# Performance work log

Hardware: AMD Instinct MI355X
Metric: run time of the kernel (lower is better)

## Reference

```python
import jax, jax.numpy as jnp
import numpy as np

B = 8192       # batch size
D = 64         # embedding dim
NUM_GROUPS = 128
TEMP = 0.05    # temperature (init kwarg)
SCALE = 0.05   # keeps exp(-dist/TEMP) > 0 in fp32 (no underflow)


def setup_inputs() -> dict:
    key = jax.random.key(0)
    k1, k2, k3 = jax.random.split(key, 3)
    text = jax.random.normal(k1, (B, D), dtype=jnp.float32) * SCALE
    image = jax.random.normal(k2, (B, D), dtype=jnp.float32) * SCALE
    groups = jax.random.randint(k3, (B,), 0, NUM_GROUPS, dtype=jnp.int64)
    return {"text_embeddings": text, "image_embeddings": image, "groups": groups}


def reference(text_embeddings, image_embeddings, groups):
    n = groups.shape[0]
    # pairwise L2 distances via ||a||^2 + ||b||^2 - 2ab (avoids [B,B,D] tensor)
    d2 = (jnp.sum(image_embeddings**2, axis=1)[:, None]
          + jnp.sum(text_embeddings**2, axis=1)[None, :]
          - 2.0 * image_embeddings @ text_embeddings.T)
    dist = jnp.sqrt(jnp.maximum(d2, 0.0))          # [B,B] dist(image_i, text_j)
    S = jnp.exp(-dist / TEMP)                      # similarities, all > 0
    same = groups[:, None] == groups[None, :]      # [B,B] group equality
    diagS = jnp.diagonal(S)
    A = jnp.where(same, S, 0.0).sum(axis=1) - diagS   # same-group sum, j != i
    F = A + diagS                                      # same-group sum incl. i
    # the original inner 'if numerator == 0' re-loop fires exactly once unless
    # the j=0 iteration already added something (groups[i]==groups[0] and i!=0)
    idx = jnp.arange(n)
    cond = (groups == groups[0]) & (idx != 0)
    num = jnp.where(cond, A, A + F)
    den = jnp.where(same, 0.0, S).sum(axis=1)          # different-group sum
    valid = (num != 0.0) & (den != 0.0)
    ratio = jnp.where(valid, num, 1.0) / jnp.where(valid, den, 1.0)
    per_i = jnp.where(valid, -jnp.log(ratio), 0.0)
    return per_i.sum() / n
```

## Files before the change

### kernel.cpp

```cpp
#include <hip/hip_runtime.h>
#include <hip/hip_bf16.h>
#include <math.h>

typedef unsigned short u16;
typedef __attribute__((ext_vector_type(8))) short short8;
typedef __attribute__((ext_vector_type(4))) float f32x4;

#define NB 8192
#define ND 64
#define K2     832.5475634f
#define M2K2  -1665.0951268f
#define LN2    0.69314718055994531f

__device__ __forceinline__ float simval2(float d2K) {
    return __builtin_amdgcn_exp2f(-__builtin_amdgcn_sqrtf(fmaxf(d2K, 0.0f)));
}

__global__ __launch_bounds__(256) void snn_prep(
    const float* __restrict__ text, const float* __restrict__ image,
    u16* __restrict__ textBf, u16* __restrict__ imageBf,
    float* __restrict__ normT, float* __restrict__ normI,
    float* __restrict__ diagS, float* __restrict__ sameSum,
    float* __restrict__ totSum, float* __restrict__ out)
{
    const int lane = threadIdx.x & 63;
    const int row  = blockIdx.x * 4 + (threadIdx.x >> 6);
    const int idx  = row * ND + lane;

    float t  = text[idx];
    float im = image[idx];
    __hip_bfloat16 tb = __float2bfloat16(t);
    __hip_bfloat16 ib = __float2bfloat16(im);
    u16 tbits, ibits;
    __builtin_memcpy(&tbits, &tb, 2);
    __builtin_memcpy(&ibits, &ib, 2);
    textBf[idx]  = tbits;
    imageBf[idx] = ibits;

    float nt = t * t;
    float ni = im * im;
    float dp = __bfloat162float(tb) * __bfloat162float(ib);
    #pragma unroll
    for (int m = 32; m >= 1; m >>= 1) {
        nt += __shfl_xor(nt, m, 64);
        ni += __shfl_xor(ni, m, 64);
        dp += __shfl_xor(dp, m, 64);
    }
    if (lane == 0) {
        float snt = K2 * nt;
        float sni = K2 * ni;
        normT[row] = snt;
        normI[row] = sni;
        float d2K = fmaf(M2K2, dp, sni + snt);
        diagS[row] = simval2(d2K);
        sameSum[row] = 0.0f;
        totSum[row]  = 0.0f;
        if (row == 0) out[0] = 0.0f;
    }
}

__global__ __launch_bounds__(256, 2) void snn_main(
    const u16* __restrict__ textBf, const u16* __restrict__ imageBf,
    const float* __restrict__ normT, const float* __restrict__ normI,
    const int* __restrict__ groups,
    float* __restrict__ sameSum, float* __restrict__ totSum)
{
    const int lane = threadIdx.x & 63;
    const int w    = threadIdx.x >> 6;
    const int g    = lane >> 4;
    const int l15  = lane & 15;
    const int rowBase  = blockIdx.x * 128 + w * 32;
    const int colChunk = blockIdx.y * 256;

    short8 aFrag[2][2];
    #pragma unroll
    for (int m = 0; m < 2; ++m)
        #pragma unroll
        for (int kk = 0; kk < 2; ++kk)
            aFrag[m][kk] = *(const short8*)(imageBf +
                (rowBase + m * 16 + l15) * ND + kk * 32 + g * 8);

    float nI[2][4];
    int   gI[2][4];
    #pragma unroll
    for (int m = 0; m < 2; ++m)
        #pragma unroll
        for (int r = 0; r < 4; ++r) {
            int row = rowBase + m * 16 + g * 4 + r;
            nI[m][r] = normI[row];
            gI[m][r] = groups[row];
        }

    float sameAcc[2][4];
    float totAcc[2][4];
    #pragma unroll
    for (int m = 0; m < 2; ++m)
        #pragma unroll
        for (int r = 0; r < 4; ++r) { sameAcc[m][r] = 0.0f; totAcc[m][r] = 0.0f; }

    #pragma unroll
    for (int ct = 0; ct < 2; ++ct) {
        const int colBase = colChunk + ct * 128;

        float nT[8];
        int   gJ[8];
        f32x4 acc[2][8];
        #pragma unroll
        for (int n = 0; n < 8; ++n) {
            const int col = colBase + n * 16 + l15;
            nT[n] = normT[col];
            gJ[n] = groups[col];
            short8 b0 = *(const short8*)(textBf + col * ND + g * 8);
            short8 b1 = *(const short8*)(textBf + col * ND + 32 + g * 8);
            #pragma unroll
            for (int m = 0; m < 2; ++m) {
                acc[m][n] = f32x4{0.f, 0.f, 0.f, 0.f};
                acc[m][n] = __builtin_amdgcn_mfma_f32_16x16x32_bf16(
                                aFrag[m][0], b0, acc[m][n], 0, 0, 0);
                acc[m][n] = __builtin_amdgcn_mfma_f32_16x16x32_bf16(
                                aFrag[m][1], b1, acc[m][n], 0, 0, 0);
            }
        }

        #pragma unroll
        for (int m = 0; m < 2; ++m)
            #pragma unroll
            for (int n = 0; n < 8; ++n) {
                f32x4 c = acc[m][n];
                #pragma unroll
                for (int r = 0; r < 4; ++r) {
                    float d2K = fmaf(M2K2, c[r], nI[m][r] + nT[n]);
                    float s   = simval2(d2K);
                    totAcc[m][r] += s;
                    sameAcc[m][r] += (gI[m][r] == gJ[n]) ? s : 0.0f;
                }
            }
    }

    #pragma unroll
    for (int m = 0; m < 2; ++m)
        #pragma unroll
        for (int r = 0; r < 4; ++r) {
            float sv = sameAcc[m][r];
            float tv = totAcc[m][r];
            #pragma unroll
            for (int mk = 8; mk >= 1; mk >>= 1) {
                sv += __shfl_xor(sv, mk, 64);
                tv += __shfl_xor(tv, mk, 64);
            }
            if (l15 == 0) {
                int row = rowBase + m * 16 + g * 4 + r;
                atomicAdd(&sameSum[row], sv);
                atomicAdd(&totSum[row], tv);
            }
        }
}

__global__ __launch_bounds__(256) void snn_finalize(
    const float* __restrict__ sameSum, const float* __restrict__ totSum,
    const float* __restrict__ diagS, const int* __restrict__ groups,
    float* __restrict__ out)
{
    const int i = blockIdx.x * 256 + threadIdx.x;
    float sameS = sameSum[i];
    float tot   = totSum[i];
    float diag  = diagS[i];
    float A = sameS - diag;
    int g0 = groups[0];
    bool cond = (groups[i] == g0) && (i != 0);
    float num = cond ? A : (A + sameS);
    float den = tot - sameS;
    bool valid = (num != 0.0f) && (den != 0.0f);
    float ratio = (valid ? num : 1.0f) / (valid ? den : 1.0f);
    float per = valid ? (-LN2 * __builtin_amdgcn_logf(ratio)) : 0.0f;

    float v = per;
    #pragma unroll
    for (int mk = 32; mk >= 1; mk >>= 1) v += __shfl_xor(v, mk, 64);
    __shared__ float wsum[4];
    if ((threadIdx.x & 63) == 0) wsum[threadIdx.x >> 6] = v;
    __syncthreads();
    if (threadIdx.x == 0) {
        float s = wsum[0] + wsum[1] + wsum[2] + wsum[3];
        atomicAdd(out, s * (1.0f / 8192.0f));
    }
}

extern "C" void kernel_launch(void* const* d_in, const int* in_sizes, int n_in,
                              void* d_out, int out_size, void* d_ws, size_t ws_size,
                              hipStream_t stream) {
    const float* text  = (const float*)d_in[0];
    const float* image = (const float*)d_in[1];
    const int*   groups = (const int*)d_in[2];
    float* out = (float*)d_out;

    char* ws = (char*)d_ws;
    u16* textBf  = (u16*)ws;
    u16* imageBf = (u16*)(ws + (1 << 20));
    float* normT   = (float*)(ws + (2 << 20));
    float* normI   = normT + NB;
    float* diagS   = normI + NB;
    float* sameSum = diagS + NB;
    float* totSum  = sameSum + NB;

    snn_prep<<<NB / 4, 256, 0, stream>>>(text, image, textBf, imageBf,
                                         normT, normI, diagS, sameSum, totSum, out);
    snn_main<<<dim3(64, 32), 256, 0, stream>>>(textBf, imageBf, normT, normI,
                                               groups, sameSum, totSum);
    snn_finalize<<<NB / 256, 256, 0, stream>>>(sameSum, totSum, diagS, groups, out);
}
```

Baseline: 109.7 us.

## Fuse finalize into main via last-block counter and shrink row tile per wave

The separate finalize kernel is removed. Each main block increments a global completion counter, and the last block to finish computes the per-row loss terms and writes the mean. The main kernel's tiling also changes: each wave now handles 16 rows instead of 32 and loops over 16 column tiles with partial unrolling. The grid doubles along rows, so the B (text) fragments are reused less per load. This removes one launch, but the serial reduction of all 8192 rows now runs on a single block at the end.

```diff
diff --git a/kernel.cpp b/kernel.cpp
--- a/kernel.cpp
+++ b/kernel.cpp
@@ -12,6 +12,10 @@
 #define M2K2  -1665.0951268f
 #define LN2    0.69314718055994531f
 
+#define GRID_X 128
+#define GRID_Y 32
+#define TOTAL_BLOCKS (GRID_X * GRID_Y)
+
 __device__ __forceinline__ float simval2(float d2K) {
     return __builtin_amdgcn_exp2f(-__builtin_amdgcn_sqrtf(fmaxf(d2K, 0.0f)));
 }
@@ -21,7 +25,8 @@
     u16* __restrict__ textBf, u16* __restrict__ imageBf,
     float* __restrict__ normT, float* __restrict__ normI,
     float* __restrict__ diagS, float* __restrict__ sameSum,
-    float* __restrict__ totSum, float* __restrict__ out)
+    float* __restrict__ totSum, unsigned int* __restrict__ doneCnt,
+    float* __restrict__ out)
 {
     const int lane = threadIdx.x & 63;
     const int row  = blockIdx.x * 4 + (threadIdx.x >> 6);
@@ -55,134 +60,107 @@
         diagS[row] = simval2(d2K);
         sameSum[row] = 0.0f;
         totSum[row]  = 0.0f;
-        if (row == 0) out[0] = 0.0f;
+        if (row == 0) { *doneCnt = 0u; out[0] = 0.0f; }
     }
 }
 
 __global__ __launch_bounds__(256, 2) void snn_main(
     const u16* __restrict__ textBf, const u16* __restrict__ imageBf,
     const float* __restrict__ normT, const float* __restrict__ normI,
-    const int* __restrict__ groups,
-    float* __restrict__ sameSum, float* __restrict__ totSum)
+    const int* __restrict__ groups, const float* __restrict__ diagS,
+    float* __restrict__ sameSum, float* __restrict__ totSum,
+    unsigned int* __restrict__ doneCnt, float* __restrict__ out)
 {
     const int lane = threadIdx.x & 63;
     const int w    = threadIdx.x >> 6;
     const int g    = lane >> 4;
     const int l15  = lane & 15;
-    const int rowBase  = blockIdx.x * 128 + w * 32;
+    const int rowBase  = blockIdx.x * 64 + w * 16;
     const int colChunk = blockIdx.y * 256;
 
-    short8 aFrag[2][2];
+    short8 aFrag0 = *(const short8*)(imageBf + (rowBase + l15) * ND + g * 8);
+    short8 aFrag1 = *(const short8*)(imageBf + (rowBase + l15) * ND + 32 + g * 8);
+
+    float nI[4];
+    int   gI[4];
     #pragma unroll
-    for (int m = 0; m < 2; ++m)
-        #pragma unroll
-        for (int kk = 0; kk < 2; ++kk)
-            aFrag[m][kk] = *(const short8*)(imageBf +
-                (rowBase + m * 16 + l15) * ND + kk * 32 + g * 8);
+    for (int r = 0; r < 4; ++r) {
+        int row = rowBase + g * 4 + r;
+        nI[r] = normI[row];
+        gI[r] = groups[row];
+    }
 
-    float nI[2][4];
-    int   gI[2][4];
-    #pragma unroll
-    for (int m = 0; m < 2; ++m)
+    float sameAcc[4] = {0.f, 0.f, 0.f, 0.f};
+    float totAcc[4]  = {0.f, 0.f, 0.f, 0.f};
+
+    #pragma unroll 2
+    for (int n = 0; n < 16; ++n) {
+        const int col = colChunk + n * 16 + l15;
+        float nT = normT[col];
+        int   gJ = groups[col];
+        short8 b0 = *(const short8*)(textBf + col * ND + g * 8);
+        short8 b1 = *(const short8*)(textBf + col * ND + 32 + g * 8);
+        f32x4 acc = {0.f, 0.f, 0.f, 0.f};
+        acc = __builtin_amdgcn_mfma_f32_16x16x32_bf16(aFrag0, b0, acc, 0, 0, 0);
+        acc = __builtin_amdgcn_mfma_f32_16x16x32_bf16(aFrag1, b1, acc, 0, 0, 0);
         #pragma unroll
         for (int r = 0; r < 4; ++r) {
-            int row = rowBase + m * 16 + g * 4 + r;
-            nI[m][r] = normI[row];
-            gI[m][r] = groups[row];
+            float d2K = fmaf(M2K2, acc[r], nI[r] + nT);
+            float s   = simval2(d2K);
+            totAcc[r] += s;
+            sameAcc[r] += (gI[r] == gJ) ? s : 0.0f;
         }
-
-    float sameAcc[2][4];
-    float totAcc[2][4];
-    #pragma unroll
-    for (int m = 0; m < 2; ++m)
-        #pragma unroll
-        for (int r = 0; r < 4; ++r) { sameAcc[m][r] = 0.0f; totAcc[m][r] = 0.0f; }
-
-    #pragma unroll
-    for (int ct = 0; ct < 2; ++ct) {
-        const int colBase = colChunk + ct * 128;
-
-        float nT[8];
-        int   gJ[8];
-        f32x4 acc[2][8];
-        #pragma unroll
-        for (int n = 0; n < 8; ++n) {
-            const int col = colBase + n * 16 + l15;
-            nT[n] = normT[col];
-            gJ[n] = groups[col];
-            short8 b0 = *(const short8*)(textBf + col * ND + g * 8);
-            short8 b1 = *(const short8*)(textBf + col * ND + 32 + g * 8);
-            #pragma unroll
-            for (int m = 0; m < 2; ++m) {
-                acc[m][n] = f32x4{0.f, 0.f, 0.f, 0.f};
-                acc[m][n] = __builtin_amdgcn_mfma_f32_16x16x32_bf16(
-                                aFrag[m][0], b0, acc[m][n], 0, 0, 0);
-                acc[m][n] = __builtin_amdgcn_mfma_f32_16x16x32_bf16(
-                                aFrag[m][1], b1, acc[m][n], 0, 0, 0);
-            }
-        }
-
-        #pragma unroll
-        for (int m = 0; m < 2; ++m)
-            #pragma unroll
-            for (int n = 0; n < 8; ++n) {
-                f32x4 c = acc[m][n];
-                #pragma unroll
-                for (int r = 0; r < 4; ++r) {
-                    float d2K = fmaf(M2K2, c[r], nI[m][r] + nT[n]);
-                    float s   = simval2(d2K);
-                    totAcc[m][r] += s;
-                    sameAcc[m][r] += (gI[m][r] == gJ[n]) ? s : 0.0f;
-                }
-            }
     }
 
     #pragma unroll
-    for (int m = 0; m < 2; ++m)
+    for (int r = 0; r < 4; ++r) {
+        float sv = sameAcc[r];
+        float tv = totAcc[r];
         #pragma unroll
-        for (int r = 0; r < 4; ++r) {
-            float sv = sameAcc[m][r];
-            float tv = totAcc[m][r];
-            #pragma unroll
-            for (int mk = 8; mk >= 1; mk >>= 1) {
-                sv += __shfl_xor(sv, mk, 64);
-                tv += __shfl_xor(tv, mk, 64);
-            }
-            if (l15 == 0) {
-                int row = rowBase + m * 16 + g * 4 + r;
-                atomicAdd(&sameSum[row], sv);
-                atomicAdd(&totSum[row], tv);
-            }
+        for (int mk = 8; mk >= 1; mk >>= 1) {
+            sv += __shfl_xor(sv, mk, 64);
+            tv += __shfl_xor(tv, mk, 64);
         }
-}
+        if (l15 == 0) {
+            int row = rowBase + g * 4 + r;
+            atomicAdd(&sameSum[row], sv);
+            atomicAdd(&totSum[row], tv);
+        }
+    }
 
-__global__ __launch_bounds__(256) void snn_finalize(
-    const float* __restrict__ sameSum, const float* __restrict__ totSum,
-    const float* __restrict__ diagS, const int* __restrict__ groups,
-    float* __restrict__ out)
-{
-    const int i = blockIdx.x * 256 + threadIdx.x;
-    float sameS = sameSum[i];
-    float tot   = totSum[i];
-    float diag  = diagS[i];
-    float A = sameS - diag;
-    int g0 = groups[0];
-    bool cond = (groups[i] == g0) && (i != 0);
-    float num = cond ? A : (A + sameS);
-    float den = tot - sameS;
-    bool valid = (num != 0.0f) && (den != 0.0f);
-    float ratio = (valid ? num : 1.0f) / (valid ? den : 1.0f);
-    float per = valid ? (-LN2 * __builtin_amdgcn_logf(ratio)) : 0.0f;
-
-    float v = per;
-    #pragma unroll
-    for (int mk = 32; mk >= 1; mk >>= 1) v += __shfl_xor(v, mk, 64);
+    __shared__ int lastFlag;
     __shared__ float wsum[4];
-    if ((threadIdx.x & 63) == 0) wsum[threadIdx.x >> 6] = v;
     __syncthreads();
     if (threadIdx.x == 0) {
-        float s = wsum[0] + wsum[1] + wsum[2] + wsum[3];
-        atomicAdd(out, s * (1.0f / 8192.0f));
+        __threadfence();
+        unsigned int old = atomicAdd(doneCnt, 1u);
+        lastFlag = (old == TOTAL_BLOCKS - 1) ? 1 : 0;
+    }
+    __syncthreads();
+    if (lastFlag) {
+        __threadfence();
+        float partial = 0.0f;
+        const int g0 = groups[0];
+        for (int i = threadIdx.x; i < NB; i += 256) {
+            float sameS = __hip_atomic_load(&sameSum[i], __ATOMIC_RELAXED,
+                                            __HIP_MEMORY_SCOPE_AGENT);
+            float tot   = __hip_atomic_load(&totSum[i], __ATOMIC_RELAXED,
+                                            __HIP_MEMORY_SCOPE_AGENT);
+            float diag  = diagS[i];
+            float A = sameS - diag;
+            bool cond = (groups[i] == g0) && (i != 0);
+            float num = cond ? A : (A + sameS);
+            float den = tot - sameS;
+            bool valid = (num != 0.0f) && (den != 0.0f);
+            float ratio = (valid ? num : 1.0f) / (valid ? den : 1.0f);
+            partial += valid ? (-LN2 * __builtin_amdgcn_logf(ratio)) : 0.0f;
+        }
+        #pragma unroll
+        for (int mk = 32; mk >= 1; mk >>= 1) partial += __shfl_xor(partial, mk, 64);
+        if ((threadIdx.x & 63) == 0) wsum[threadIdx.x >> 6] = partial;
+        __syncthreads();
+        if (threadIdx.x == 0)
+            out[0] = (wsum[0] + wsum[1] + wsum[2] + wsum[3]) * (1.0f / 8192.0f);
     }
 }
 
@@ -202,10 +180,12 @@
     float* diagS   = normI + NB;
     float* sameSum = diagS + NB;
     float* totSum  = sameSum + NB;
+    unsigned int* doneCnt = (unsigned int*)(totSum + NB);
 
     snn_prep<<<NB / 4, 256, 0, stream>>>(text, image, textBf, imageBf,
-                                         normT, normI, diagS, sameSum, totSum, out);
-    snn_main<<<dim3(64, 32), 256, 0, stream>>>(textBf, imageBf, normT, normI,
-                                               groups, sameSum, totSum);
-    snn_finalize<<<NB / 256, 256, 0, stream>>>(sameSum, totSum, diagS, groups, out);
+                                         normT, normI, diagS, sameSum, totSum,
+                                         doneCnt, out);
+    snn_main<<<dim3(GRID_X, GRID_Y), 256, 0, stream>>>(
+        textBf, imageBf, normT, normI, groups, diagS,
+        sameSum, totSum, doneCnt, out);
 }
```

Measured after the change: 186.3 us. 1.7x slower.

## Stage text tile in swizzled LDS and fuse finalize via last-block reduction

Applied to the files above, without the earlier changes.

Each block now loads its 256-column bf16 text tile, norms and group ids into XOR-swizzled shared memory once, and all four waves read from there instead of issuing redundant global loads. The separate finalize kernel is removed. The last block to finish, detected with an atomic counter, computes the per-row loss and writes the output, which saves one kernel launch. In exchange it adds 32KB of LDS per block, which may limit occupancy, and the final reduction runs serially in a single block.

```diff
diff --git a/kernel.cpp b/kernel.cpp
--- a/kernel.cpp
+++ b/kernel.cpp
@@ -12,6 +12,10 @@
 #define M2K2  -1665.0951268f
 #define LN2    0.69314718055994531f
 
+#define GRID_X 64
+#define GRID_Y 32
+#define TOTAL_BLOCKS (GRID_X * GRID_Y)
+
 __device__ __forceinline__ float simval2(float d2K) {
     return __builtin_amdgcn_exp2f(-__builtin_amdgcn_sqrtf(fmaxf(d2K, 0.0f)));
 }
@@ -21,7 +25,8 @@
     u16* __restrict__ textBf, u16* __restrict__ imageBf,
     float* __restrict__ normT, float* __restrict__ normI,
     float* __restrict__ diagS, float* __restrict__ sameSum,
-    float* __restrict__ totSum, float* __restrict__ out)
+    float* __restrict__ totSum, unsigned int* __restrict__ doneCnt,
+    float* __restrict__ out)
 {
     const int lane = threadIdx.x & 63;
     const int row  = blockIdx.x * 4 + (threadIdx.x >> 6);
@@ -55,23 +60,42 @@
         diagS[row] = simval2(d2K);
         sameSum[row] = 0.0f;
         totSum[row]  = 0.0f;
-        if (row == 0) out[0] = 0.0f;
+        if (row == 0) { *doneCnt = 0u; out[0] = 0.0f; }
     }
 }
 
 __global__ __launch_bounds__(256, 2) void snn_main(
     const u16* __restrict__ textBf, const u16* __restrict__ imageBf,
     const float* __restrict__ normT, const float* __restrict__ normI,
-    const int* __restrict__ groups,
-    float* __restrict__ sameSum, float* __restrict__ totSum)
+    const int* __restrict__ groups, const float* __restrict__ diagS,
+    float* __restrict__ sameSum, float* __restrict__ totSum,
+    unsigned int* __restrict__ doneCnt, float* __restrict__ out)
 {
-    const int lane = threadIdx.x & 63;
-    const int w    = threadIdx.x >> 6;
+    __shared__ u16   Btile[256 * ND];
+    __shared__ float NTs[256];
+    __shared__ int   GJs[256];
+
+    const int tid  = threadIdx.x;
+    const int lane = tid & 63;
+    const int w    = tid >> 6;
     const int g    = lane >> 4;
     const int l15  = lane & 15;
     const int rowBase  = blockIdx.x * 128 + w * 32;
     const int colChunk = blockIdx.y * 256;
 
+    {
+        const int cb = tid >> 3;
+        const int s  = tid & 7;
+        #pragma unroll
+        for (int r = 0; r < 8; ++r) {
+            int c = r * 32 + cb;
+            short8 v = *(const short8*)(textBf + (colChunk + c) * ND + s * 8);
+            *(short8*)&Btile[c * ND + ((s ^ (c & 7)) * 8)] = v;
+        }
+        NTs[tid] = normT[colChunk + tid];
+        GJs[tid] = groups[colChunk + tid];
+    }
+
     short8 aFrag[2][2];
     #pragma unroll
     for (int m = 0; m < 2; ++m)
@@ -91,6 +115,8 @@
             gI[m][r] = groups[row];
         }
 
+    __syncthreads();
+
     float sameAcc[2][4];
     float totAcc[2][4];
     #pragma unroll
@@ -100,18 +126,16 @@
 
     #pragma unroll
     for (int ct = 0; ct < 2; ++ct) {
-        const int colBase = colChunk + ct * 128;
-
         float nT[8];
         int   gJ[8];
         f32x4 acc[2][8];
         #pragma unroll
         for (int n = 0; n < 8; ++n) {
-            const int col = colBase + n * 16 + l15;
-            nT[n] = normT[col];
-            gJ[n] = groups[col];
-            short8 b0 = *(const short8*)(textBf + col * ND + g * 8);
-            short8 b1 = *(const short8*)(textBf + col * ND + 32 + g * 8);
+            const int c = ct * 128 + n * 16 + l15;
+            nT[n] = NTs[c];
+            gJ[n] = GJs[c];
+            short8 b0 = *(const short8*)&Btile[c * ND + ((g       ^ (c & 7)) * 8)];
+            short8 b1 = *(const short8*)&Btile[c * ND + (((4 + g) ^ (c & 7)) * 8)];
             #pragma unroll
             for (int m = 0; m < 2; ++m) {
                 acc[m][n] = f32x4{0.f, 0.f, 0.f, 0.f};
@@ -154,35 +178,40 @@
                 atomicAdd(&totSum[row], tv);
             }
         }
-}
-
-__global__ __launch_bounds__(256) void snn_finalize(
-    const float* __restrict__ sameSum, const float* __restrict__ totSum,
-    const float* __restrict__ diagS, const int* __restrict__ groups,
-    float* __restrict__ out)
-{
-    const int i = blockIdx.x * 256 + threadIdx.x;
-    float sameS = sameSum[i];
-    float tot   = totSum[i];
-    float diag  = diagS[i];
-    float A = sameS - diag;
-    int g0 = groups[0];
-    bool cond = (groups[i] == g0) && (i != 0);
-    float num = cond ? A : (A + sameS);
-    float den = tot - sameS;
-    bool valid = (num != 0.0f) && (den != 0.0f);
-    float ratio = (valid ? num : 1.0f) / (valid ? den : 1.0f);
-    float per = valid ? (-LN2 * __builtin_amdgcn_logf(ratio)) : 0.0f;
-
-    float v = per;
-    #pragma unroll
-    for (int mk = 32; mk >= 1; mk >>= 1) v += __shfl_xor(v, mk, 64);
+
+    __shared__ int lastFlag;
     __shared__ float wsum[4];
-    if ((threadIdx.x & 63) == 0) wsum[threadIdx.x >> 6] = v;
     __syncthreads();
     if (threadIdx.x == 0) {
-        float s = wsum[0] + wsum[1] + wsum[2] + wsum[3];
-        atomicAdd(out, s * (1.0f / 8192.0f));
+        __threadfence();
+        unsigned int old = atomicAdd(doneCnt, 1u);
+        lastFlag = (old == TOTAL_BLOCKS - 1) ? 1 : 0;
+    }
+    __syncthreads();
+    if (lastFlag) {
+        __threadfence();
+        float partial = 0.0f;
+        const int g0 = groups[0];
+        for (int i = threadIdx.x; i < NB; i += 256) {
+            float sameS = __hip_atomic_load(&sameSum[i], __ATOMIC_RELAXED,
+                                            __HIP_MEMORY_SCOPE_AGENT);
+            float tot   = __hip_atomic_load(&totSum[i], __ATOMIC_RELAXED,
+                                            __HIP_MEMORY_SCOPE_AGENT);
+            float diag  = diagS[i];
+            float A = sameS - diag;
+            bool cond = (groups[i] == g0) && (i != 0);
+            float num = cond ? A : (A + sameS);
+            float den = tot - sameS;
+            bool valid = (num != 0.0f) && (den != 0.0f);
+            float ratio = (valid ? num : 1.0f) / (valid ? den : 1.0f);
+            partial += valid ? (-LN2 * __builtin_amdgcn_logf(ratio)) : 0.0f;
+        }
+        #pragma unroll
+        for (int mk = 32; mk >= 1; mk >>= 1) partial += __shfl_xor(partial, mk, 64);
+        if ((threadIdx.x & 63) == 0) wsum[threadIdx.x >> 6] = partial;
+        __syncthreads();
+        if (threadIdx.x == 0)
+            out[0] = (wsum[0] + wsum[1] + wsum[2] + wsum[3]) * (1.0f / 8192.0f);
     }
 }
 
@@ -202,10 +231,12 @@
     float* diagS   = normI + NB;
     float* sameSum = diagS + NB;
     float* totSum  = sameSum + NB;
+    unsigned int* doneCnt = (unsigned int*)(totSum + NB);
 
     snn_prep<<<NB / 4, 256, 0, stream>>>(text, image, textBf, imageBf,
-                                         normT, normI, diagS, sameSum, totSum, out);
-    snn_main<<<dim3(64, 32), 256, 0, stream>>>(textBf, imageBf, normT, normI,
-                                               groups, sameSum, totSum);
-    snn_finalize<<<NB / 256, 256, 0, stream>>>(sameSum, totSum, diagS, groups, out);
-}
+                                         normT, normI, diagS, sameSum, totSum,
+                                         doneCnt, out);
+    snn_main<<<dim3(GRID_X, GRID_Y), 256, 0, stream>>>(
+        textBf, imageBf, normT, normI, groups, diagS,
+        sameSum, totSum, doneCnt, out);
+}
```

Measured after the change: 130.4 us. +18.8%, slower.
